# Kernel tuning notes

Measured on AMD Instinct MI355X. Metric: run time of the kernel, lower is better.

## Reference

```python
import jax, jax.numpy as jnp
import numpy as np

S = 4096          # seq_len (longformer-large-4096)
H = 1024          # hidden_size
FF = 3072         # ffnn_size (hardcoded)
G = 100           # number of gold mentions
MAX_SPAN = 30     # max_span_length
TOP_LAMBDA = 0.2
LN_EPS = 1e-5
MASK_VAL = 10000.0


def setup_inputs() -> dict:
    key = jax.random.key(0)
    ks = jax.random.split(key, 16)
    sc = 0.02
    sequence_output = jax.random.normal(ks[0], (1, S, H), jnp.float32)
    attention_mask = jnp.ones((1, S), jnp.int32)
    # valid gold spans: 1 <= start <= end < start + MAX_SPAN (so torch's >0 filter keeps all)
    gs = jax.random.randint(ks[1], (G,), 1, S - MAX_SPAN)
    gl = jax.random.randint(ks[2], (G,), 0, MAX_SPAN)
    gold_mentions = jnp.stack([gs, gs + gl], axis=1).astype(jnp.int32)  # [G, 2]
    inp = {
        'sequence_output': sequence_output,
        'attention_mask': attention_mask,
        'gold_mentions': gold_mentions,
        # start_mention_mlp
        'W_sm': jax.random.normal(ks[3], (H, FF), jnp.float32) * sc,
        'b_sm': jnp.zeros((FF,), jnp.float32),
        'g_sm': jnp.ones((FF,), jnp.float32),
        'beta_sm': jnp.zeros((FF,), jnp.float32),
        # end_mention_mlp
        'W_em': jax.random.normal(ks[4], (H, FF), jnp.float32) * sc,
        'b_em': jnp.zeros((FF,), jnp.float32),
        'g_em': jnp.ones((FF,), jnp.float32),
        'beta_em': jnp.zeros((FF,), jnp.float32),
        # classifiers
        'w_start': jax.random.normal(ks[5], (FF,), jnp.float32) * sc,
        'b_start': jnp.zeros((), jnp.float32),
        'w_end': jax.random.normal(ks[6], (FF,), jnp.float32) * sc,
        'b_end': jnp.zeros((), jnp.float32),
        'W_s2e': jax.random.normal(ks[7], (FF, FF), jnp.float32) * sc,
        'b_s2e': jnp.zeros((FF,), jnp.float32),
    }
    return inp


def _fcl(x, W, b, g, beta):
    # dense -> gelu (exact) -> layernorm (dropout is identity in eval)
    h = jax.nn.gelu(x @ W + b, approximate=False)
    mu = jnp.mean(h, axis=-1, keepdims=True)
    var = jnp.mean(jnp.square(h - mu), axis=-1, keepdims=True)
    return (h - mu) * jax.lax.rsqrt(var + LN_EPS) * g + beta


def _forward(sequence_output, attention_mask, gold_mentions,
             W_sm, b_sm, g_sm, beta_sm, W_em, b_em, g_em, beta_em,
             w_start, b_start, w_end, b_end, W_s2e, b_s2e):
    start_reps = _fcl(sequence_output, W_sm, b_sm, g_sm, beta_sm)  # [1,S,FF]
    end_reps = _fcl(sequence_output, W_em, b_em, g_em, beta_em)    # [1,S,FF]

    start_logits = jnp.einsum('bsf,f->bs', start_reps, w_start) + b_start  # [1,S]
    end_logits = jnp.einsum('bsf,f->bs', end_reps, w_end) + b_end          # [1,S]
    temp = start_reps @ W_s2e + b_s2e                                      # [1,S,FF]
    joint = jnp.einsum('bsf,btf->bst', temp, end_reps)                     # [1,S,S]
    mention_logits = joint + start_logits[:, :, None] + end_logits[:, None, :]

    # span mask: start <= end < start + MAX_SPAN (triu(0) then tril(MAX_SPAN-1))
    i = jnp.arange(S)
    mention_mask = ((i[:, None] <= i[None, :]) & (i[None, :] < i[:, None] + MAX_SPAN)
                    ).astype(jnp.float32)[None]  # [1,S,S]
    mention_logits = jnp.clip(mention_logits + (1.0 - mention_mask) * (-MASK_VAL),
                              -MASK_VAL, MASK_VAL)

    # top-k pruning; attention_mask is full so k is static: int(S * 0.2)
    max_k = int(S * TOP_LAMBDA)  # 819
    _, topk_1d = jax.lax.top_k(mention_logits.reshape(1, -1), max_k)  # [1,max_k]
    sorted_idx = jnp.sort(topk_1d, axis=-1)
    topk_start_ids = sorted_idx // S
    topk_end_ids = sorted_idx % S
    span_mask = jnp.ones((1, max_k), jnp.float32)

    # losses
    probs = jax.nn.sigmoid(mention_logits)  # [1,S,S]
    gstart = gold_mentions[:, 0]
    gend = gold_mentions[:, 1]
    gold_probs = probs[0, gstart, gend]
    # torch BCE clamps log at -100
    cost_gold = -jnp.mean(jnp.maximum(jnp.log(gold_probs), -100.0))
    junk = probs.at[0, gstart, gend].set(0.0)
    log1mp = jnp.maximum(jnp.log(1.0 - junk), -100.0)
    cost_junk = -jnp.sum(jnp.where(mention_mask == 1.0, log1mp, 0.0)) / jnp.sum(mention_mask)
    cost_is_mention = (cost_gold + cost_junk)[None]  # [1]

    return topk_start_ids, topk_end_ids, span_mask, sequence_output, cost_is_mention


def reference(sequence_output, attention_mask, gold_mentions,
              W_sm, b_sm, g_sm, beta_sm, W_em, b_em, g_em, beta_em,
              w_start, b_start, w_end, b_end, W_s2e, b_s2e):
    return _forward(sequence_output, attention_mask, gold_mentions,
                    W_sm, b_sm, g_sm, beta_sm, W_em, b_em, g_em, beta_em,
                    w_start, b_start, w_end, b_end, W_s2e, b_s2e)
```

## Files before the change

### kernel.cpp

```cpp
#include <hip/hip_runtime.h>
#include <math.h>

#define S 4096
#define H 1024
#define FF 3072
#define G 100
#define MAXSPAN 30
#define MAXK 819
#define NBAND (S * MAXSPAN)
#define BAND_COUNT 122445.0

#define O_START 0
#define O_END   819
#define O_MASK  1638
#define O_SEQ   2457
#define O_COST  (2457 + S * H)

typedef __bf16 bf16x8 __attribute__((ext_vector_type(8)));
typedef float f32x4 __attribute__((ext_vector_type(4)));
typedef float f32x16 __attribute__((ext_vector_type(16)));


__device__ __forceinline__ float block_reduce_256(float x, volatile float* red) {
  #pragma unroll
  for (int off = 32; off > 0; off >>= 1) x += __shfl_down(x, off, 64);
  int wid = threadIdx.x >> 6;
  int lane = threadIdx.x & 63;
  __syncthreads();
  if (lane == 0) red[wid] = x;
  __syncthreads();
  return red[0] + red[1] + red[2] + red[3];
}

__device__ __forceinline__ unsigned f2key(float f) {
  unsigned b = __float_as_uint(f);
  return (b & 0x80000000u) ? ~b : (b | 0x80000000u);
}

__device__ __forceinline__ unsigned short bf16_rne(float x) {
  unsigned u = __float_as_uint(x);
  unsigned r = ((u >> 16) & 1u) + 0x7FFFu;
  return (unsigned short)((u + r) >> 16);
}

__device__ __forceinline__ void split2(float x, unsigned short& h, unsigned short& l) {
  h = bf16_rne(x);
  float hf = __uint_as_float(((unsigned)h) << 16);
  l = bf16_rne(x - hf);
}

__device__ __forceinline__ void gld16(const void* g, void* l) {
  __builtin_amdgcn_global_load_lds(
      (const __attribute__((address_space(1))) unsigned int*)g,
      (__attribute__((address_space(3))) unsigned int*)l, 16, 0, 0);
}


__global__ __launch_bounds__(256) void pack_a_kernel(const float* __restrict__ A,
                                                     unsigned short* __restrict__ hi,
                                                     unsigned short* __restrict__ lo,
                                                     int K) {
  __shared__ float tile[32][33];
  const int t = threadIdx.x;
  const int tx = t & 31, ty8 = t >> 5;
  const int k0 = blockIdx.x * 32, r0 = blockIdx.y * 32;
  #pragma unroll
  for (int r = ty8; r < 32; r += 8)
    tile[r][tx] = A[(size_t)(r0 + r) * K + k0 + tx];
  __syncthreads();
  if (t < 128) {
    const int kql = t >> 5;
    const int rl = t & 31;
    unsigned short h8[8], l8[8];
    #pragma unroll
    for (int s = 0; s < 8; s++) split2(tile[rl][kql * 8 + s], h8[s], l8[s]);
    const size_t panel = (size_t)(r0 >> 7);
    const int rloc = (r0 & 127) + rl;
    const size_t off = panel * (size_t)(128 * K) + (size_t)(k0 / 8 + kql) * 1024 + (size_t)rloc * 8;
    *(uint4*)(hi + off) = *(const uint4*)h8;
    *(uint4*)(lo + off) = *(const uint4*)l8;
  }
}

__global__ __launch_bounds__(256) void pack_ln_a_kernel(const float* __restrict__ A,
                                                        const float* __restrict__ mu,
                                                        const float* __restrict__ rstd,
                                                        const float* __restrict__ g,
                                                        const float* __restrict__ beta,
                                                        unsigned short* __restrict__ hi,
                                                        unsigned short* __restrict__ lo,
                                                        int K) {
  __shared__ float tile[32][33];
  const int t = threadIdx.x;
  const int tx = t & 31, ty8 = t >> 5;
  const int k0 = blockIdx.x * 32, r0 = blockIdx.y * 32;
  #pragma unroll
  for (int r = ty8; r < 32; r += 8)
    tile[r][tx] = A[(size_t)(r0 + r) * K + k0 + tx];
  __syncthreads();
  if (t < 128) {
    const int kql = t >> 5;
    const int rl = t & 31;
    const int row = r0 + rl;
    const float m = mu[row], rs = rstd[row];
    float4 g0 = *(const float4*)(g + k0 + kql * 8);
    float4 g1 = *(const float4*)(g + k0 + kql * 8 + 4);
    float4 b0 = *(const float4*)(beta + k0 + kql * 8);
    float4 b1 = *(const float4*)(beta + k0 + kql * 8 + 4);
    float gv[8] = {g0.x, g0.y, g0.z, g0.w, g1.x, g1.y, g1.z, g1.w};
    float bv[8] = {b0.x, b0.y, b0.z, b0.w, b1.x, b1.y, b1.z, b1.w};
    unsigned short h8[8], l8[8];
    #pragma unroll
    for (int s = 0; s < 8; s++) {
      float v = (tile[rl][kql * 8 + s] - m) * rs * gv[s] + bv[s];
      split2(v, h8[s], l8[s]);
    }
    const size_t panel = (size_t)(r0 >> 7);
    const int rloc = (r0 & 127) + rl;
    const size_t off = panel * (size_t)(128 * K) + (size_t)(k0 / 8 + kql) * 1024 + (size_t)rloc * 8;
    *(uint4*)(hi + off) = *(const uint4*)h8;
    *(uint4*)(lo + off) = *(const uint4*)l8;
  }
}

__global__ __launch_bounds__(256) void pack_bt_kernel(const float* __restrict__ W,
                                                      unsigned short* __restrict__ hi,
                                                      unsigned short* __restrict__ lo,
                                                      int K, int N) {
  __shared__ float tile[32][33];
  const int t = threadIdx.x;
  const int tx = t & 31, ty8 = t >> 5;
  const int k0 = blockIdx.x * 32, n0 = blockIdx.y * 32;
  #pragma unroll
  for (int r = ty8; r < 32; r += 8)
    tile[r][tx] = W[(size_t)(k0 + r) * N + n0 + tx];
  __syncthreads();
  if (t < 128) {
    const int kql = t >> 5;
    const int nl = t & 31;
    unsigned short h8[8], l8[8];
    #pragma unroll
    for (int s = 0; s < 8; s++) split2(tile[kql * 8 + s][nl], h8[s], l8[s]);
    const size_t panel = (size_t)(n0 >> 7);
    const int nloc = (n0 & 127) + nl;
    const size_t off = panel * (size_t)(128 * K) + (size_t)(k0 / 8 + kql) * 1024 + (size_t)nloc * 8;
    *(uint4*)(hi + off) = *(const uint4*)h8;
    *(uint4*)(lo + off) = *(const uint4*)l8;
  }
}


template <int EPI>
__device__ __forceinline__ void gemm_body(const char* cAh, const char* cAl,
                                          const char* cBh, const char* cBl,
                                          const float* __restrict__ bias,
                                          float* __restrict__ C,
                                          int bm, int bn, int N, int K,
                                          char* smem) {
  const int tid = threadIdx.x;
  const int lane = tid & 63;
  const int wid = __builtin_amdgcn_readfirstlane(tid >> 6);
  const int wm = wid >> 1, wn = wid & 1;
  const int lb = lane * 16;
  const int ldsq = wid * 2048;

  const int khalf = lane >> 5;
  const int r31 = lane & 31;
  const int abase = khalf * 2048 + (wm * 64 + r31) * 16;
  const int bbase = khalf * 2048 + (wn * 64 + r31) * 16;

  f32x16 acc[2][2];
  #pragma unroll
  for (int a = 0; a < 2; a++)
    #pragma unroll
    for (int b = 0; b < 2; b++)
      #pragma unroll
      for (int r = 0; r < 16; r++) acc[a][b][r] = 0.0f;

  for (int k0 = 0; k0 < K; k0 += 32) {
    const size_t qb = (size_t)((k0 >> 3) + wid) * 2048 + lb;
    __syncthreads();
    gld16(cAh + qb,        smem +     0 + ldsq);
    gld16(cAh + qb + 1024, smem +     0 + ldsq + 1024);
    gld16(cAl + qb,        smem +  8192 + ldsq);
    gld16(cAl + qb + 1024, smem +  8192 + ldsq + 1024);
    gld16(cBh + qb,        smem + 16384 + ldsq);
    gld16(cBh + qb + 1024, smem + 16384 + ldsq + 1024);
    gld16(cBl + qb,        smem + 24576 + ldsq);
    gld16(cBl + qb + 1024, smem + 24576 + ldsq + 1024);
    __syncthreads();

    bf16x8 ah[2][2], al[2][2], bh[2][2], bl[2][2];
    #pragma unroll
    for (int ks = 0; ks < 2; ks++) {
      #pragma unroll
      for (int mt = 0; mt < 2; mt++) {
        ah[ks][mt] = *(const bf16x8*)(smem +     0 + ks * 4096 + abase + mt * 512);
        al[ks][mt] = *(const bf16x8*)(smem +  8192 + ks * 4096 + abase + mt * 512);
      }
      #pragma unroll
      for (int nt = 0; nt < 2; nt++) {
        bh[ks][nt] = *(const bf16x8*)(smem + 16384 + ks * 4096 + bbase + nt * 512);
        bl[ks][nt] = *(const bf16x8*)(smem + 24576 + ks * 4096 + bbase + nt * 512);
      }
    }
    #pragma unroll
    for (int ks = 0; ks < 2; ks++)
      #pragma unroll
      for (int mt = 0; mt < 2; mt++)
        #pragma unroll
        for (int nt = 0; nt < 2; nt++) {
          acc[mt][nt] = __builtin_amdgcn_mfma_f32_32x32x16_bf16(ah[ks][mt], bh[ks][nt], acc[mt][nt], 0, 0, 0);
          acc[mt][nt] = __builtin_amdgcn_mfma_f32_32x32x16_bf16(al[ks][mt], bh[ks][nt], acc[mt][nt], 0, 0, 0);
          acc[mt][nt] = __builtin_amdgcn_mfma_f32_32x32x16_bf16(ah[ks][mt], bl[ks][nt], acc[mt][nt], 0, 0, 0);
        }
  }

  #pragma unroll
  for (int mt = 0; mt < 2; mt++) {
    #pragma unroll
    for (int nt = 0; nt < 2; nt++) {
      const int colg = bn + wn * 64 + nt * 32 + r31;
      const float bb = bias[colg];
      #pragma unroll
      for (int reg = 0; reg < 16; reg++) {
        const int rowl = (reg & 3) + 8 * (reg >> 2) + 4 * khalf;
        const int rowg = bm + wm * 64 + mt * 32 + rowl;
        float v = acc[mt][nt][reg] + bb;
        if (EPI == 1) v = 0.5f * v * (1.0f + erff(v * 0.70710678118654752f));
        C[(size_t)rowg * N + colg] = v;
      }
    }
  }
}

__global__ __launch_bounds__(256) void gemm_mfma_kernel(const unsigned short* __restrict__ Ahi,
                                                        const unsigned short* __restrict__ Alo,
                                                        const unsigned short* __restrict__ Bhi,
                                                        const unsigned short* __restrict__ Blo,
                                                        const float* __restrict__ bias,
                                                        float* __restrict__ C,
                                                        int N, int K) {
  __shared__ __align__(16) char smem[32768];
  const size_t panAb = (size_t)blockIdx.y * (size_t)(128 * K) * 2;
  const size_t panBb = (size_t)blockIdx.x * (size_t)(128 * K) * 2;
  gemm_body<0>((const char*)Ahi + panAb, (const char*)Alo + panAb,
               (const char*)Bhi + panBb, (const char*)Blo + panBb,
               bias, C, blockIdx.y * 128, blockIdx.x * 128, N, K, smem);
}

__global__ __launch_bounds__(256) void gemm_mfma_dual_kernel(const unsigned short* __restrict__ Ahi,
                                                             const unsigned short* __restrict__ Alo,
                                                             const unsigned short* __restrict__ B1hi,
                                                             const unsigned short* __restrict__ B1lo,
                                                             const unsigned short* __restrict__ B2hi,
                                                             const unsigned short* __restrict__ B2lo,
                                                             const float* __restrict__ bias1,
                                                             const float* __restrict__ bias2,
                                                             float* __restrict__ C1,
                                                             float* __restrict__ C2,
                                                             int N, int K) {
  __shared__ __align__(16) char smem[32768];
  const int zb = blockIdx.z;
  const unsigned short* Bhi = zb ? B2hi : B1hi;
  const unsigned short* Blo = zb ? B2lo : B1lo;
  const float* bias = zb ? bias2 : bias1;
  float* C = zb ? C2 : C1;
  const size_t panAb = (size_t)blockIdx.y * (size_t)(128 * K) * 2;
  const size_t panBb = (size_t)blockIdx.x * (size_t)(128 * K) * 2;
  gemm_body<1>((const char*)Ahi + panAb, (const char*)Alo + panAb,
               (const char*)Bhi + panBb, (const char*)Blo + panBb,
               bias, C, blockIdx.y * 128, blockIdx.x * 128, N, K, smem);
}


__global__ __launch_bounds__(256) void ln_stats_kernel(const float* __restrict__ HbS,
                                                       const float* __restrict__ HbE,
                                                       const float* __restrict__ gS,
                                                       const float* __restrict__ betaS,
                                                       const float* __restrict__ wS,
                                                       const float* __restrict__ bS,
                                                       const float* __restrict__ gE,
                                                       const float* __restrict__ betaE,
                                                       const float* __restrict__ wE,
                                                       const float* __restrict__ bE,
                                                       float* __restrict__ slog,
                                                       float* __restrict__ elog,
                                                       float* __restrict__ muS,
                                                       float* __restrict__ rstdS,
                                                       float* __restrict__ muE,
                                                       float* __restrict__ rstdE) {
  __shared__ float red[4];
  const int row = blockIdx.x, tid = threadIdx.x;
  const int br = blockIdx.y;
  const float* Hb = br ? HbE : HbS;
  const float* g = br ? gE : gS;
  const float* beta = br ? betaE : betaS;
  const float* w = br ? wE : wS;
  const float* bsc = br ? bE : bS;
  const float* h = Hb + (size_t)row * FF;

  float4 v[3];
  float s = 0.0f;
  #pragma unroll
  for (int t = 0; t < 3; t++) {
    v[t] = *(const float4*)(h + tid * 4 + t * 1024);
    s += v[t].x + v[t].y + v[t].z + v[t].w;
  }
  float mu = block_reduce_256(s, red) * (1.0f / (float)FF);

  float s2 = 0.0f;
  #pragma unroll
  for (int t = 0; t < 3; t++) {
    float dx = v[t].x - mu, dy = v[t].y - mu, dz = v[t].z - mu, dw = v[t].w - mu;
    s2 += dx * dx + dy * dy + dz * dz + dw * dw;
  }
  float var = block_reduce_256(s2, red) * (1.0f / (float)FF);
  float rstd = rsqrtf(var + 1e-5f);

  float dot = 0.0f;
  #pragma unroll
  for (int t = 0; t < 3; t++) {
    int idx = tid * 4 + t * 1024;
    float4 gv = *(const float4*)(g + idx);
    float4 bv = *(const float4*)(beta + idx);
    float4 wv = *(const float4*)(w + idx);
    float rx = (v[t].x - mu) * rstd * gv.x + bv.x;
    float ry = (v[t].y - mu) * rstd * gv.y + bv.y;
    float rz = (v[t].z - mu) * rstd * gv.z + bv.z;
    float rw = (v[t].w - mu) * rstd * gv.w + bv.w;
    dot += rx * wv.x + ry * wv.y + rz * wv.z + rw * wv.w;
  }
  float dt = block_reduce_256(dot, red);
  if (tid == 0) {
    if (br) { elog[row] = dt + bsc[0]; muE[row] = mu; rstdE[row] = rstd; }
    else    { slog[row] = dt + bsc[0]; muS[row] = mu; rstdS[row] = rstd; }
  }
}


__global__ __launch_bounds__(256) void band_joint_kernel(const float* __restrict__ T,
                                                         const float* __restrict__ Eraw,
                                                         const float* __restrict__ muE,
                                                         const float* __restrict__ rstdE,
                                                         const float* __restrict__ gE,
                                                         const float* __restrict__ betaE,
                                                         const float* __restrict__ sl,
                                                         const float* __restrict__ el,
                                                         float* __restrict__ band) {
  __shared__ float Elds[45][260];
  const int t = threadIdx.x;
  const int bx = blockIdx.x;
  const int sbx = (bx & 7) * 32 + (bx >> 3);
  const int i0 = sbx * 16;
  const int r_l = t >> 4, c = t & 15;

  float accd[MAXSPAN];
  #pragma unroll
  for (int d = 0; d < MAXSPAN; d++) accd[d] = 0.0f;

  for (int k0 = 0; k0 < FF; k0 += 256) {
    const float* trow = T + (size_t)(i0 + r_l) * FF + k0 + c * 16;
    float4 tv0 = *(const float4*)(trow + 0);
    float4 tv1 = *(const float4*)(trow + 4);
    float4 tv2 = *(const float4*)(trow + 8);
    float4 tv3 = *(const float4*)(trow + 12);
    __syncthreads();
    for (int rr = t >> 6; rr < 45; rr += 4) {
      int gr = i0 + rr;
      int cc = (t & 63) * 4;
      float4 rv = {0.f, 0.f, 0.f, 0.f};
      if (gr < S) {
        float4 ev = *(const float4*)(Eraw + (size_t)gr * FF + k0 + cc);
        float m = muE[gr], rs = rstdE[gr];
        float4 gv = *(const float4*)(gE + k0 + cc);
        float4 bv = *(const float4*)(betaE + k0 + cc);
        rv.x = (ev.x - m) * rs * gv.x + bv.x;
        rv.y = (ev.y - m) * rs * gv.y + bv.y;
        rv.z = (ev.z - m) * rs * gv.z + bv.z;
        rv.w = (ev.w - m) * rs * gv.w + bv.w;
      }
      *(float4*)&Elds[rr][cc] = rv;
    }
    __syncthreads();
    #pragma unroll
    for (int d = 0; d < MAXSPAN; d++) {
      const float* er = &Elds[r_l + d][c * 16];
      float4 e0 = *(const float4*)(er + 0);
      float4 e1 = *(const float4*)(er + 4);
      float4 e2 = *(const float4*)(er + 8);
      float4 e3 = *(const float4*)(er + 12);
      accd[d] += tv0.x * e0.x + tv0.y * e0.y + tv0.z * e0.z + tv0.w * e0.w
               + tv1.x * e1.x + tv1.y * e1.y + tv1.z * e1.z + tv1.w * e1.w
               + tv2.x * e2.x + tv2.y * e2.y + tv2.z * e2.z + tv2.w * e2.w
               + tv3.x * e3.x + tv3.y * e3.y + tv3.z * e3.z + tv3.w * e3.w;
    }
  }

  const int i = i0 + r_l;
  const float my_sl = sl[i];
  #pragma unroll
  for (int d = 0; d < MAXSPAN; d++) {
    float v = accd[d];
    v += __shfl_down(v, 8, 16);
    v += __shfl_down(v, 4, 16);
    v += __shfl_down(v, 2, 16);
    v += __shfl_down(v, 1, 16);
    if (c == 0) {
      int j = i + d;
      if (j < S) {
        float vv = v + my_sl + el[j];
        vv = fminf(fmaxf(vv, -10000.0f), 10000.0f);
        band[i * MAXSPAN + d] = vv;
      } else {
        band[i * MAXSPAN + d] = -1e30f;
      }
    }
  }
}


__global__ void mark_gold_kernel(const int* __restrict__ gold, char* __restrict__ mark) {
  int t = threadIdx.x;
  if (t < G) {
    int gs = gold[2 * t], ge = gold[2 * t + 1];
    mark[gs * MAXSPAN + (ge - gs)] = 1;
  }
}

__global__ __launch_bounds__(256) void cost_junk_kernel(const float* __restrict__ band,
                                                        const char* __restrict__ mark,
                                                        double* __restrict__ jacc) {
  __shared__ float red[4];
  int e = blockIdx.x * 256 + threadIdx.x;
  int i = e / MAXSPAN, d = e - i * MAXSPAN;
  float term = 0.0f;
  if (i + d < S && !mark[e]) {
    float x = band[e];
    float p = 1.0f / (1.0f + expf(-x));
    term = fmaxf(logf(1.0f - p), -100.0f);
  }
  float ssum = block_reduce_256(term, red);
  if (threadIdx.x == 0) atomicAdd(jacc, (double)ssum);
}

__global__ __launch_bounds__(256) void finalize_kernel(const float* __restrict__ band,
                                                       const int* __restrict__ gold,
                                                       const double* __restrict__ jacc,
                                                       float* __restrict__ outc) {
  __shared__ float red[4];
  int t = threadIdx.x;
  float term = 0.0f;
  if (t < G) {
    int gs = gold[2 * t], ge = gold[2 * t + 1];
    float x = band[gs * MAXSPAN + (ge - gs)];
    float p = 1.0f / (1.0f + expf(-x));
    term = fmaxf(logf(p), -100.0f);
  }
  float sg = block_reduce_256(term, red);
  if (t == 0) {
    double cost = -((double)sg / (double)G) - ((*jacc) / BAND_COUNT);
    *outc = (float)cost;
  }
}


__global__ __launch_bounds__(1024) void topk_kernel(const float* __restrict__ band,
                                                    float* __restrict__ out) {
  __shared__ int hist[256];
  __shared__ unsigned sh_prefix;
  __shared__ int sh_remk;
  __shared__ int idxbuf[1024];
  __shared__ unsigned tkey[256];
  __shared__ int tidx[256];
  __shared__ int cnt_gt, cnt_eq;
  __shared__ int sb[1024];
  const int tid = threadIdx.x;

  if (tid < 256) hist[tid] = 0;
  __syncthreads();
  for (int e = tid; e < NBAND; e += 1024)
    atomicAdd(&hist[f2key(band[e]) >> 24], 1);
  __syncthreads();
  if (tid == 0) {
    int cum = 0, b = 255;
    for (; b > 0; b--) {
      if (cum + hist[b] >= MAXK) break;
      cum += hist[b];
    }
    sh_prefix = (unsigned)b;
    sh_remk = MAXK - cum;
  }
  __syncthreads();
  const unsigned p8 = sh_prefix;
  int remk = sh_remk;
  __syncthreads();

  if (tid < 256) hist[tid] = 0;
  __syncthreads();
  for (int e = tid; e < NBAND; e += 1024) {
    unsigned key = f2key(band[e]);
    if ((key >> 24) == p8) atomicAdd(&hist[(key >> 16) & 255], 1);
  }
  __syncthreads();
  if (tid == 0) {
    int cum = 0, b = 255;
    for (; b > 0; b--) {
      if (cum + hist[b] >= remk) break;
      cum += hist[b];
    }
    sh_prefix = (p8 << 8) | (unsigned)b;
    sh_remk = remk - cum;
  }
  __syncthreads();
  const unsigned T16 = sh_prefix;
  remk = sh_remk;

  if (tid == 0) { cnt_gt = 0; cnt_eq = 0; }
  __syncthreads();
  for (int e = tid; e < NBAND; e += 1024) {
    unsigned key = f2key(band[e]);
    unsigned k16 = key >> 16;
    if (k16 >= T16) {
      int i = e / MAXSPAN, d = e - i * MAXSPAN;
      int fi = i * S + i + d;
      if (k16 > T16) {
        int p = atomicAdd(&cnt_gt, 1);
        if (p < 1024) idxbuf[p] = fi;
      } else {
        int p = atomicAdd(&cnt_eq, 1);
        if (p < 256) { tkey[p] = key; tidx[p] = fi; }
      }
    }
  }
  __syncthreads();
  if (tid == 0) {
    int ngt = cnt_gt < 1024 ? cnt_gt : 1024;
    int ne = cnt_eq < 256 ? cnt_eq : 256;
    for (int a2 = 1; a2 < ne; a2++) {
      unsigned kv = tkey[a2]; int iv = tidx[a2];
      int b2 = a2 - 1;
      while (b2 >= 0 && (tkey[b2] < kv || (tkey[b2] == kv && tidx[b2] > iv))) {
        tkey[b2 + 1] = tkey[b2]; tidx[b2 + 1] = tidx[b2]; b2--;
      }
      tkey[b2 + 1] = kv; tidx[b2 + 1] = iv;
    }
    int take = remk < ne ? remk : ne;
    for (int q = 0; q < take; q++)
      if (ngt + q < 1024) idxbuf[ngt + q] = tidx[q];
  }
  __syncthreads();

  sb[tid] = (tid < MAXK) ? idxbuf[tid] : 0x7FFFFFFF;
  __syncthreads();
  for (int ksz = 2; ksz <= 1024; ksz <<= 1) {
    for (int jj = ksz >> 1; jj > 0; jj >>= 1) {
      int ixj = tid ^ jj;
      if (ixj > tid) {
        int a2 = sb[tid], b2 = sb[ixj];
        bool up = ((tid & ksz) == 0);
        if (up ? (a2 > b2) : (a2 < b2)) { sb[tid] = b2; sb[ixj] = a2; }
      }
      __syncthreads();
    }
  }
  if (tid < MAXK) {
    int fi = sb[tid];
    out[O_START + tid] = (float)(fi >> 12);
    out[O_END + tid]   = (float)(fi & 4095);
    out[O_MASK + tid]  = 1.0f;
  }
}


extern "C" void kernel_launch(void* const* d_in, const int* in_sizes, int n_in,
                              void* d_out, int out_size, void* d_ws, size_t ws_size,
                              hipStream_t stream) {
  (void)in_sizes; (void)n_in; (void)out_size; (void)ws_size;
  const float* seq    = (const float*)d_in[0];
  const int*   gold   = (const int*)d_in[2];
  const float* W_sm   = (const float*)d_in[3];
  const float* b_sm   = (const float*)d_in[4];
  const float* g_sm   = (const float*)d_in[5];
  const float* be_sm  = (const float*)d_in[6];
  const float* W_em   = (const float*)d_in[7];
  const float* b_em   = (const float*)d_in[8];
  const float* g_em   = (const float*)d_in[9];
  const float* be_em  = (const float*)d_in[10];
  const float* w_st   = (const float*)d_in[11];
  const float* b_st   = (const float*)d_in[12];
  const float* w_en   = (const float*)d_in[13];
  const float* b_en   = (const float*)d_in[14];
  const float* W_s2e  = (const float*)d_in[15];
  const float* b_s2e  = (const float*)d_in[16];
  float* out = (float*)d_out;
  char* ws = (char*)d_ws;

  const size_t SZ_REP = (size_t)S * FF * 4;
  float*  bufS = (float*)(ws);
  float*  bufE = (float*)(ws + SZ_REP);
  float*  bufT = (float*)(ws + 2 * SZ_REP);
  char* R3 = ws + 3 * SZ_REP;
  unsigned short* seqhi = (unsigned short*)R3;
  unsigned short* seqlo = (unsigned short*)(R3 + (size_t)S * H * 2);
  unsigned short* a3hi  = (unsigned short*)R3;
  unsigned short* a3lo  = (unsigned short*)(R3 + (size_t)S * FF * 2);
  char* R4 = ws + 4 * SZ_REP;
  const size_t SZ_W12 = (size_t)H * FF * 2;
  unsigned short* wb1hi = (unsigned short*)R4;
  unsigned short* wb1lo = (unsigned short*)(R4 + SZ_W12);
  unsigned short* wb2hi = (unsigned short*)(R4 + 2 * SZ_W12);
  unsigned short* wb2lo = (unsigned short*)(R4 + 3 * SZ_W12);
  unsigned short* wbhi = (unsigned short*)R4;
  unsigned short* wblo = (unsigned short*)(R4 + (size_t)FF * FF * 2);
  char* R5 = R4 + 2 * (size_t)FF * FF * 2;
  float*  band = (float*)R5;
  char*   mark = R5 + (size_t)NBAND * 4;
  double* jacc = (double*)(R5 + (size_t)NBAND * 4 + NBAND + 32);
  float*  slog = (float*)(R5 + (size_t)NBAND * 4 + NBAND + 128);
  float*  elog  = slog + S;
  float*  muS   = elog + S;
  float*  rstdS = muS + S;
  float*  muE   = rstdS + S;
  float*  rstdE = muE + S;

  hipMemsetAsync(mark, 0, NBAND, stream);
  hipMemsetAsync(jacc, 0, 8, stream);

  dim3 gg(FF / 128, S / 128);
  dim3 gg2(FF / 128, S / 128, 2);

  pack_a_kernel<<<dim3(H / 32, S / 32), 256, 0, stream>>>(seq, seqhi, seqlo, H);
  pack_bt_kernel<<<dim3(H / 32, FF / 32), 256, 0, stream>>>(W_sm, wb1hi, wb1lo, H, FF);
  pack_bt_kernel<<<dim3(H / 32, FF / 32), 256, 0, stream>>>(W_em, wb2hi, wb2lo, H, FF);
  gemm_mfma_dual_kernel<<<gg2, 256, 0, stream>>>(seqhi, seqlo, wb1hi, wb1lo, wb2hi, wb2lo,
                                                 b_sm, b_em, bufS, bufE, FF, H);
  ln_stats_kernel<<<dim3(S, 2), 256, 0, stream>>>(bufS, bufE, g_sm, be_sm, w_st, b_st,
                                                  g_em, be_em, w_en, b_en,
                                                  slog, elog, muS, rstdS, muE, rstdE);
  pack_ln_a_kernel<<<dim3(FF / 32, S / 32), 256, 0, stream>>>(bufS, muS, rstdS, g_sm, be_sm, a3hi, a3lo, FF);
  pack_bt_kernel<<<dim3(FF / 32, FF / 32), 256, 0, stream>>>(W_s2e, wbhi, wblo, FF, FF);
  gemm_mfma_kernel<<<gg, 256, 0, stream>>>(a3hi, a3lo, wbhi, wblo, b_s2e, bufT, FF, FF);

  band_joint_kernel<<<S / 16, 256, 0, stream>>>(bufT, bufE, muE, rstdE, g_em, be_em,
                                                slog, elog, band);

  mark_gold_kernel<<<1, 128, 0, stream>>>(gold, mark);
  cost_junk_kernel<<<NBAND / 256, 256, 0, stream>>>(band, mark, jacc);
  topk_kernel<<<1, 1024, 0, stream>>>(band, out);
  finalize_kernel<<<1, 256, 0, stream>>>(band, gold, jacc, out + O_COST);

  hipMemcpyAsync(out + O_SEQ, seq, (size_t)S * H * 4, hipMemcpyDeviceToDevice, stream);
}
```

Baseline: 824.3 us.

## Fuse layernorm statistics into GEMM epilogue and merge loss/topk kernels

The dual GEMM epilogue now accumulates per-row sum, sum of squares and the gamma*w weighted dot with warp shuffles and atomics. A small finalize kernel then derives the mean, rstd and logits algebraically, which removes the separate full pass over both FF-wide activations. The junk-cost reduction moves into the band kernel, the gold-cell correction and final cost fold into the topk kernel, and the two weight packs merge into one launch, so several launches and memsets disappear. The trade-offs are atomic contention, a one-pass variance that is less numerically stable, and float atomics that make the reduction order nondeterministic.

```diff
diff --git a/kernel.cpp b/kernel.cpp
--- a/kernel.cpp
+++ b/kernel.cpp
@@ -17,7 +17,6 @@
 #define O_COST  (2457 + S * H)
 
 typedef __bf16 bf16x8 __attribute__((ext_vector_type(8)));
-typedef float f32x4 __attribute__((ext_vector_type(4)));
 typedef float f32x16 __attribute__((ext_vector_type(16)));
 
 
@@ -30,6 +29,20 @@
   if (lane == 0) red[wid] = x;
   __syncthreads();
   return red[0] + red[1] + red[2] + red[3];
+}
+
+__device__ __forceinline__ float block_reduce_1024(float x, volatile float* red) {
+  #pragma unroll
+  for (int off = 32; off > 0; off >>= 1) x += __shfl_down(x, off, 64);
+  int wid = threadIdx.x >> 6;
+  int lane = threadIdx.x & 63;
+  __syncthreads();
+  if (lane == 0) red[wid] = x;
+  __syncthreads();
+  float s = 0.f;
+  #pragma unroll
+  for (int q = 0; q < 16; q++) s += red[q];
+  return s;
 }
 
 __device__ __forceinline__ unsigned f2key(float f) {
@@ -53,6 +66,22 @@
   __builtin_amdgcn_global_load_lds(
       (const __attribute__((address_space(1))) unsigned int*)g,
       (__attribute__((address_space(3))) unsigned int*)l, 16, 0, 0);
+}
+
+
+__global__ __launch_bounds__(256) void prep_kernel(const float* __restrict__ g_sm,
+                                                   const float* __restrict__ w_st,
+                                                   const float* __restrict__ g_em,
+                                                   const float* __restrict__ w_en,
+                                                   float* __restrict__ gwS,
+                                                   float* __restrict__ gwE,
+                                                   float* __restrict__ sums,
+                                                   double* __restrict__ jacc) {
+  int i = blockIdx.x * 256 + threadIdx.x;
+  if (i < FF) gwS[i] = g_sm[i] * w_st[i];
+  else if (i < 2 * FF) gwE[i - FF] = g_em[i - FF] * w_en[i - FF];
+  if (i < 6 * S) sums[i] = 0.0f;
+  if (i == 0) *jacc = 0.0;
 }
 
 
@@ -123,10 +152,10 @@
   }
 }
 
-__global__ __launch_bounds__(256) void pack_bt_kernel(const float* __restrict__ W,
-                                                      unsigned short* __restrict__ hi,
-                                                      unsigned short* __restrict__ lo,
-                                                      int K, int N) {
+__device__ __forceinline__ void pack_bt_body(const float* __restrict__ W,
+                                             unsigned short* __restrict__ hi,
+                                             unsigned short* __restrict__ lo,
+                                             int K, int N) {
   __shared__ float tile[32][33];
   const int t = threadIdx.x;
   const int tx = t & 31, ty8 = t >> 5;
@@ -149,12 +178,32 @@
   }
 }
 
+__global__ __launch_bounds__(256) void pack_bt_kernel(const float* __restrict__ W,
+                                                      unsigned short* __restrict__ hi,
+                                                      unsigned short* __restrict__ lo,
+                                                      int K, int N) {
+  pack_bt_body(W, hi, lo, K, N);
+}
+
+__global__ __launch_bounds__(256) void pack_bt_dual_kernel(const float* __restrict__ W1,
+                                                           const float* __restrict__ W2,
+                                                           unsigned short* __restrict__ h1,
+                                                           unsigned short* __restrict__ l1,
+                                                           unsigned short* __restrict__ h2,
+                                                           unsigned short* __restrict__ l2,
+                                                           int K, int N) {
+  if (blockIdx.z == 0) pack_bt_body(W1, h1, l1, K, N);
+  else                 pack_bt_body(W2, h2, l2, K, N);
+}
+
 
 template <int EPI>
 __device__ __forceinline__ void gemm_body(const char* cAh, const char* cAl,
                                           const char* cBh, const char* cBl,
                                           const float* __restrict__ bias,
                                           float* __restrict__ C,
+                                          const float* __restrict__ gw,
+                                          float* __restrict__ sums,
                                           int bm, int bn, int N, int K,
                                           char* smem) {
   const int tid = threadIdx.x;
@@ -216,6 +265,11 @@
         }
   }
 
+  float gwc[2];
+  if (EPI == 1) {
+    gwc[0] = gw[bn + wn * 64 + r31];
+    gwc[1] = gw[bn + wn * 64 + 32 + r31];
+  }
   #pragma unroll
   for (int mt = 0; mt < 2; mt++) {
     #pragma unroll
@@ -227,8 +281,35 @@
         const int rowl = (reg & 3) + 8 * (reg >> 2) + 4 * khalf;
         const int rowg = bm + wm * 64 + mt * 32 + rowl;
         float v = acc[mt][nt][reg] + bb;
-        if (EPI == 1) v = 0.5f * v * (1.0f + erff(v * 0.70710678118654752f));
+        if (EPI == 1) {
+          v = 0.5f * v * (1.0f + erff(v * 0.70710678118654752f));
+          acc[mt][nt][reg] = v;
+        }
         C[(size_t)rowg * N + colg] = v;
+      }
+    }
+  }
+  if (EPI == 1) {
+    #pragma unroll
+    for (int mt = 0; mt < 2; mt++) {
+      #pragma unroll
+      for (int reg = 0; reg < 16; reg++) {
+        float v0 = acc[mt][0][reg], v1 = acc[mt][1][reg];
+        float h = v0 + v1;
+        float h2 = v0 * v0 + v1 * v1;
+        float hw = v0 * gwc[0] + v1 * gwc[1];
+        #pragma unroll
+        for (int off = 16; off > 0; off >>= 1) {
+          h  += __shfl_down(h,  off, 32);
+          h2 += __shfl_down(h2, off, 32);
+          hw += __shfl_down(hw, off, 32);
+        }
+        if (r31 == 0) {
+          const int rowg = bm + wm * 64 + mt * 32 + (reg & 3) + 8 * (reg >> 2) + 4 * khalf;
+          atomicAdd(&sums[rowg], h);
+          atomicAdd(&sums[S + rowg], h2);
+          atomicAdd(&sums[2 * S + rowg], hw);
+        }
       }
     }
   }
@@ -246,7 +327,8 @@
   const size_t panBb = (size_t)blockIdx.x * (size_t)(128 * K) * 2;
   gemm_body<0>((const char*)Ahi + panAb, (const char*)Alo + panAb,
                (const char*)Bhi + panBb, (const char*)Blo + panBb,
-               bias, C, blockIdx.y * 128, blockIdx.x * 128, N, K, smem);
+               bias, C, nullptr, nullptr,
+               blockIdx.y * 128, blockIdx.x * 128, N, K, smem);
 }
 
 __global__ __launch_bounds__(256) void gemm_mfma_dual_kernel(const unsigned short* __restrict__ Ahi,
@@ -259,83 +341,63 @@
                                                              const float* __restrict__ bias2,
                                                              float* __restrict__ C1,
                                                              float* __restrict__ C2,
+                                                             const float* __restrict__ gwS,
+                                                             const float* __restrict__ gwE,
+                                                             float* __restrict__ sums,
                                                              int N, int K) {
   __shared__ __align__(16) char smem[32768];
   const int zb = blockIdx.z;
   const unsigned short* Bhi = zb ? B2hi : B1hi;
   const unsigned short* Blo = zb ? B2lo : B1lo;
   const float* bias = zb ? bias2 : bias1;
+  const float* gw = zb ? gwE : gwS;
   float* C = zb ? C2 : C1;
+  float* sb = sums + (zb ? 3 * S : 0);
   const size_t panAb = (size_t)blockIdx.y * (size_t)(128 * K) * 2;
   const size_t panBb = (size_t)blockIdx.x * (size_t)(128 * K) * 2;
   gemm_body<1>((const char*)Ahi + panAb, (const char*)Alo + panAb,
                (const char*)Bhi + panBb, (const char*)Blo + panBb,
-               bias, C, blockIdx.y * 128, blockIdx.x * 128, N, K, smem);
-}
-
-
-__global__ __launch_bounds__(256) void ln_stats_kernel(const float* __restrict__ HbS,
-                                                       const float* __restrict__ HbE,
-                                                       const float* __restrict__ gS,
-                                                       const float* __restrict__ betaS,
-                                                       const float* __restrict__ wS,
-                                                       const float* __restrict__ bS,
-                                                       const float* __restrict__ gE,
-                                                       const float* __restrict__ betaE,
-                                                       const float* __restrict__ wE,
-                                                       const float* __restrict__ bE,
-                                                       float* __restrict__ slog,
-                                                       float* __restrict__ elog,
-                                                       float* __restrict__ muS,
-                                                       float* __restrict__ rstdS,
-                                                       float* __restrict__ muE,
-                                                       float* __restrict__ rstdE) {
+               bias, C, gw, sb,
+               blockIdx.y * 128, blockIdx.x * 128, N, K, smem);
+}
+
+
+__global__ __launch_bounds__(256) void ln_finalize_kernel(const float* __restrict__ sums,
+                                                          const float* __restrict__ gwS,
+                                                          const float* __restrict__ beS,
+                                                          const float* __restrict__ wS,
+                                                          const float* __restrict__ bS,
+                                                          const float* __restrict__ gwE,
+                                                          const float* __restrict__ beE,
+                                                          const float* __restrict__ wE,
+                                                          const float* __restrict__ bE,
+                                                          float* __restrict__ muS,
+                                                          float* __restrict__ rstdS,
+                                                          float* __restrict__ slog,
+                                                          float* __restrict__ muE,
+                                                          float* __restrict__ rstdE,
+                                                          float* __restrict__ elog) {
   __shared__ float red[4];
-  const int row = blockIdx.x, tid = threadIdx.x;
-  const int br = blockIdx.y;
-  const float* Hb = br ? HbE : HbS;
-  const float* g = br ? gE : gS;
-  const float* beta = br ? betaE : betaS;
+  const int br = blockIdx.y, tid = threadIdx.x;
+  const float* gw = br ? gwE : gwS;
+  const float* beta = br ? beE : beS;
   const float* w = br ? wE : wS;
   const float* bsc = br ? bE : bS;
-  const float* h = Hb + (size_t)row * FF;
-
-  float4 v[3];
-  float s = 0.0f;
-  #pragma unroll
-  for (int t = 0; t < 3; t++) {
-    v[t] = *(const float4*)(h + tid * 4 + t * 1024);
-    s += v[t].x + v[t].y + v[t].z + v[t].w;
-  }
-  float mu = block_reduce_256(s, red) * (1.0f / (float)FF);
-
-  float s2 = 0.0f;
-  #pragma unroll
-  for (int t = 0; t < 3; t++) {
-    float dx = v[t].x - mu, dy = v[t].y - mu, dz = v[t].z - mu, dw = v[t].w - mu;
-    s2 += dx * dx + dy * dy + dz * dz + dw * dw;
-  }
-  float var = block_reduce_256(s2, red) * (1.0f / (float)FF);
+  const float* sb = sums + (br ? 3 * S : 0);
+
+  float a = 0.f, b = 0.f;
+  for (int k = tid; k < FF; k += 256) { a += gw[k]; b += beta[k] * w[k]; }
+  float sgw = block_reduce_256(a, red);
+  float sbw = block_reduce_256(b, red);
+
+  const int row = blockIdx.x * 256 + tid;
+  float sh = sb[row], sh2 = sb[S + row], shw = sb[2 * S + row];
+  float mu = sh * (1.0f / (float)FF);
+  float var = fmaxf(sh2 * (1.0f / (float)FF) - mu * mu, 0.0f);
   float rstd = rsqrtf(var + 1e-5f);
-
-  float dot = 0.0f;
-  #pragma unroll
-  for (int t = 0; t < 3; t++) {
-    int idx = tid * 4 + t * 1024;
-    float4 gv = *(const float4*)(g + idx);
-    float4 bv = *(const float4*)(beta + idx);
-    float4 wv = *(const float4*)(w + idx);
-    float rx = (v[t].x - mu) * rstd * gv.x + bv.x;
-    float ry = (v[t].y - mu) * rstd * gv.y + bv.y;
-    float rz = (v[t].z - mu) * rstd * gv.z + bv.z;
-    float rw = (v[t].w - mu) * rstd * gv.w + bv.w;
-    dot += rx * wv.x + ry * wv.y + rz * wv.z + rw * wv.w;
-  }
-  float dt = block_reduce_256(dot, red);
-  if (tid == 0) {
-    if (br) { elog[row] = dt + bsc[0]; muE[row] = mu; rstdE[row] = rstd; }
-    else    { slog[row] = dt + bsc[0]; muS[row] = mu; rstdS[row] = rstd; }
-  }
+  float lg = rstd * (shw - mu * sgw) + sbw + bsc[0];
+  if (br) { muE[row] = mu; rstdE[row] = rstd; elog[row] = lg; }
+  else    { muS[row] = mu; rstdS[row] = rstd; slog[row] = lg; }
 }
 
 
@@ -347,8 +409,10 @@
                                                          const float* __restrict__ betaE,
                                                          const float* __restrict__ sl,
                                                          const float* __restrict__ el,
-                                                         float* __restrict__ band) {
+                                                         float* __restrict__ band,
+                                                         double* __restrict__ jacc) {
   __shared__ float Elds[45][260];
+  __shared__ float red[4];
   const int t = threadIdx.x;
   const int bx = blockIdx.x;
   const int sbx = (bx & 7) * 32 + (bx >> 3);
@@ -399,6 +463,7 @@
 
   const int i = i0 + r_l;
   const float my_sl = sl[i];
+  float jsum = 0.0f;
   #pragma unroll
   for (int d = 0; d < MAXSPAN; d++) {
     float v = accd[d];
@@ -412,61 +477,22 @@
         float vv = v + my_sl + el[j];
         vv = fminf(fmaxf(vv, -10000.0f), 10000.0f);
         band[i * MAXSPAN + d] = vv;
+        float p = 1.0f / (1.0f + expf(-vv));
+        jsum += fmaxf(logf(1.0f - p), -100.0f);
       } else {
         band[i * MAXSPAN + d] = -1e30f;
       }
     }
   }
-}
-
-
-__global__ void mark_gold_kernel(const int* __restrict__ gold, char* __restrict__ mark) {
-  int t = threadIdx.x;
-  if (t < G) {
-    int gs = gold[2 * t], ge = gold[2 * t + 1];
-    mark[gs * MAXSPAN + (ge - gs)] = 1;
-  }
-}
-
-__global__ __launch_bounds__(256) void cost_junk_kernel(const float* __restrict__ band,
-                                                        const char* __restrict__ mark,
-                                                        double* __restrict__ jacc) {
-  __shared__ float red[4];
-  int e = blockIdx.x * 256 + threadIdx.x;
-  int i = e / MAXSPAN, d = e - i * MAXSPAN;
-  float term = 0.0f;
-  if (i + d < S && !mark[e]) {
-    float x = band[e];
-    float p = 1.0f / (1.0f + expf(-x));
-    term = fmaxf(logf(1.0f - p), -100.0f);
-  }
-  float ssum = block_reduce_256(term, red);
-  if (threadIdx.x == 0) atomicAdd(jacc, (double)ssum);
-}
-
-__global__ __launch_bounds__(256) void finalize_kernel(const float* __restrict__ band,
-                                                       const int* __restrict__ gold,
-                                                       const double* __restrict__ jacc,
-                                                       float* __restrict__ outc) {
-  __shared__ float red[4];
-  int t = threadIdx.x;
-  float term = 0.0f;
-  if (t < G) {
-    int gs = gold[2 * t], ge = gold[2 * t + 1];
-    float x = band[gs * MAXSPAN + (ge - gs)];
-    float p = 1.0f / (1.0f + expf(-x));
-    term = fmaxf(logf(p), -100.0f);
-  }
-  float sg = block_reduce_256(term, red);
-  if (t == 0) {
-    double cost = -((double)sg / (double)G) - ((*jacc) / BAND_COUNT);
-    *outc = (float)cost;
-  }
-}
-
-
-__global__ __launch_bounds__(1024) void topk_kernel(const float* __restrict__ band,
-                                                    float* __restrict__ out) {
+  float tot = block_reduce_256(jsum, red);
+  if (t == 0) atomicAdd(jacc, (double)tot);
+}
+
+
+__global__ __launch_bounds__(1024) void topk_finalize_kernel(const float* __restrict__ band,
+                                                             const int* __restrict__ gold,
+                                                             const double* __restrict__ jacc,
+                                                             float* __restrict__ out) {
   __shared__ int hist[256];
   __shared__ unsigned sh_prefix;
   __shared__ int sh_remk;
@@ -475,6 +501,8 @@
   __shared__ int tidx[256];
   __shared__ int cnt_gt, cnt_eq;
   __shared__ int sb[1024];
+  __shared__ int gcell[G];
+  __shared__ float redf[16];
   const int tid = threadIdx.x;
 
   if (tid < 256) hist[tid] = 0;
@@ -569,6 +597,30 @@
     out[O_START + tid] = (float)(fi >> 12);
     out[O_END + tid]   = (float)(fi & 4095);
     out[O_MASK + tid]  = 1.0f;
+  }
+
+  if (tid < G) {
+    int gs = gold[2 * tid], ge = gold[2 * tid + 1];
+    gcell[tid] = gs * MAXSPAN + (ge - gs);
+  }
+  __syncthreads();
+  float tg = 0.0f, tj = 0.0f;
+  if (tid < G) {
+    int cell = gcell[tid];
+    float x = band[cell];
+    float p = 1.0f / (1.0f + expf(-x));
+    tg = fmaxf(logf(p), -100.0f);
+    bool first = true;
+    for (int q = 0; q < tid; q++)
+      if (gcell[q] == cell) { first = false; break; }
+    if (first) tj = fmaxf(logf(1.0f - p), -100.0f);
+  }
+  float sg = block_reduce_1024(tg, redf);
+  float sj = block_reduce_1024(tj, redf);
+  if (tid == 0) {
+    double junk = *jacc - (double)sj;
+    double cost = -((double)sg / (double)G) - (junk / BAND_COUNT);
+    out[O_COST] = (float)cost;
   }
 }
 
@@ -615,40 +667,37 @@
   unsigned short* wblo = (unsigned short*)(R4 + (size_t)FF * FF * 2);
   char* R5 = R4 + 2 * (size_t)FF * FF * 2;
   float*  band = (float*)R5;
-  char*   mark = R5 + (size_t)NBAND * 4;
-  double* jacc = (double*)(R5 + (size_t)NBAND * 4 + NBAND + 32);
-  float*  slog = (float*)(R5 + (size_t)NBAND * 4 + NBAND + 128);
+  double* jacc = (double*)(R5 + (size_t)NBAND * 4);
+  float*  slog = (float*)(R5 + (size_t)NBAND * 4 + 64);
   float*  elog  = slog + S;
   float*  muS   = elog + S;
   float*  rstdS = muS + S;
   float*  muE   = rstdS + S;
   float*  rstdE = muE + S;
-
-  hipMemsetAsync(mark, 0, NBAND, stream);
-  hipMemsetAsync(jacc, 0, 8, stream);
+  float*  gwS   = rstdE + S;
+  float*  gwE   = gwS + FF;
+  float*  sums  = gwE + FF;
 
   dim3 gg(FF / 128, S / 128);
   dim3 gg2(FF / 128, S / 128, 2);
 
+  prep_kernel<<<96, 256, 0, stream>>>(g_sm, w_st, g_em, w_en, gwS, gwE, sums, jacc);
   pack_a_kernel<<<dim3(H / 32, S / 32), 256, 0, stream>>>(seq, seqhi, seqlo, H);
-  pack_bt_kernel<<<dim3(H / 32, FF / 32), 256, 0, stream>>>(W_sm, wb1hi, wb1lo, H, FF);
-  pack_bt_kernel<<<dim3(H / 32, FF / 32), 256, 0, stream>>>(W_em, wb2hi, wb2lo, H, FF);
+  pack_bt_dual_kernel<<<dim3(H / 32, FF / 32, 2), 256, 0, stream>>>(W_sm, W_em,
+                                                                    wb1hi, wb1lo, wb2hi, wb2lo, H, FF);
   gemm_mfma_dual_kernel<<<gg2, 256, 0, stream>>>(seqhi, seqlo, wb1hi, wb1lo, wb2hi, wb2lo,
-                                                 b_sm, b_em, bufS, bufE, FF, H);
-  ln_stats_kernel<<<dim3(S, 2), 256, 0, stream>>>(bufS, bufE, g_sm, be_sm, w_st, b_st,
-                                                  g_em, be_em, w_en, b_en,
-                                                  slog, elog, muS, rstdS, muE, rstdE);
+                                                 b_sm, b_em, bufS, bufE, gwS, gwE, sums, FF, H);
+  ln_finalize_kernel<<<dim3(S / 256, 2), 256, 0, stream>>>(sums, gwS, be_sm, w_st, b_st,
+                                                           gwE, be_em, w_en, b_en,
+                                                           muS, rstdS, slog, muE, rstdE, elog);
   pack_ln_a_kernel<<<dim3(FF / 32, S / 32), 256, 0, stream>>>(bufS, muS, rstdS, g_sm, be_sm, a3hi, a3lo, FF);
   pack_bt_kernel<<<dim3(FF / 32, FF / 32), 256, 0, stream>>>(W_s2e, wbhi, wblo, FF, FF);
   gemm_mfma_kernel<<<gg, 256, 0, stream>>>(a3hi, a3lo, wbhi, wblo, b_s2e, bufT, FF, FF);
 
   band_joint_kernel<<<S / 16, 256, 0, stream>>>(bufT, bufE, muE, rstdE, g_em, be_em,
-                                                slog, elog, band);
-
-  mark_gold_kernel<<<1, 128, 0, stream>>>(gold, mark);
-  cost_junk_kernel<<<NBAND / 256, 256, 0, stream>>>(band, mark, jacc);
-  topk_kernel<<<1, 1024, 0, stream>>>(band, out);
-  finalize_kernel<<<1, 256, 0, stream>>>(band, gold, jacc, out + O_COST);
+                                                slog, elog, band, jacc);
+
+  topk_finalize_kernel<<<1, 1024, 0, stream>>>(band, gold, jacc, out);
 
   hipMemcpyAsync(out + O_SEQ, seq, (size_t)S * H * 4, hipMemcpyDeviceToDevice, stream);
 }
```

Measured after the change: 854.8 us. 3.7% more time.
